# Optimization experiments

Hardware: AMD Instinct MI355X
Metric: run time of the kernel (lower is better)

Reference implementation:

```python
import jax, jax.numpy as jnp
import numpy as np

B, T, C = 1024, 512, 48

def setup_inputs() -> dict:
    key = jax.random.key(0)
    k1, k2, k3 = jax.random.split(key, 3)
    potentials = jax.random.normal(k1, (B, T, C), dtype=jnp.float32)
    sequence_lengths = jax.random.randint(k2, (B, 1), 1, T).astype(jnp.int32)
    # layer weight: uniform initializer (keras default uniform is U[-0.05, 0.05])
    transitions = jax.random.uniform(k3, (C, C), dtype=jnp.float32, minval=-0.05, maxval=0.05)
    return {"potentials": potentials, "sequence_lengths": sequence_lengths, "transitions": transitions}

def reference(potentials, sequence_lengths, transitions):
    # Faithful jax port of tf.contrib.crf.crf_decode (Viterbi max-plus DP),
    # followed by one_hot as in CRFLayer.call (inference branch of in_train_phase).
    Bb, Tt, Cc = potentials.shape
    seq_len = sequence_lengths.reshape(-1)  # K.flatten

    def fwd_step(score, xs):
        # score: [B,C] viterbi scores at step t-1
        pot_t, t = xs
        total = score[:, :, None] + transitions[None]  # [B, C_prev, C_cur]
        bp = jnp.argmax(total, axis=1).astype(jnp.int32)  # [B,C] best prev tag
        new_score = jnp.max(total, axis=1) + pot_t        # [B,C]
        valid = (t < seq_len)[:, None]                    # mask steps past seq_len
        score = jnp.where(valid, new_score, score)
        bp = jnp.where(valid, bp, jnp.arange(Cc, dtype=jnp.int32)[None])
        return score, bp

    init = potentials[:, 0]                               # [B,C]
    xs = (jnp.swapaxes(potentials[:, 1:], 0, 1), jnp.arange(1, Tt))
    last_score, bps = jax.lax.scan(fwd_step, init, xs)    # bps: [T-1,B,C]

    last_tag = jnp.argmax(last_score, axis=-1).astype(jnp.int32)  # [B]

    def back_step(tag_next, bp):
        prev = jnp.take_along_axis(bp, tag_next[:, None], axis=1)[:, 0]
        return prev, tag_next

    first_tag, tags_rest = jax.lax.scan(back_step, last_tag, bps, reverse=True)
    tags = jnp.concatenate([first_tag[None], tags_rest], axis=0)  # [T,B]
    tags = jnp.swapaxes(tags, 0, 1)                               # [B,T]
    return jax.nn.one_hot(tags, Cc, dtype=potentials.dtype)       # [B,T,C]
```

## Files before the change

### kernel.cpp

```cpp
#include <hip/hip_runtime.h>

#define T_DIM 512
#define C_DIM 48
#define BPS   48
#define CH    4

#if __has_builtin(__builtin_amdgcn_readlane)
#define READLANE_I(v, l) __builtin_amdgcn_readlane((v), (l))
#else
#define READLANE_I(v, l) __shfl((v), (l), 64)
#endif

#if __has_builtin(__builtin_amdgcn_wave_barrier)
#define WAVE_SYNC() do { __asm__ __volatile__("" ::: "memory"); __builtin_amdgcn_wave_barrier(); } while (0)
#else
#define WAVE_SYNC() __asm__ __volatile__("" ::: "memory")
#endif

#define DPP_MAX_STEP(V_, CTRL_) do {                                          \
    int o_ = __builtin_amdgcn_update_dpp(__float_as_int(V_),                  \
                                         __float_as_int(V_),                  \
                                         (CTRL_), 0xF, 0xF, false);           \
    V_ = fmaxf(V_, __int_as_float(o_));                                       \
} while (0)

__device__ __forceinline__ float wave_max_f(float v) {
    DPP_MAX_STEP(v, 0x111);
    DPP_MAX_STEP(v, 0x112);
    DPP_MAX_STEP(v, 0x114);
    DPP_MAX_STEP(v, 0x118);
    DPP_MAX_STEP(v, 0x142);
    DPP_MAX_STEP(v, 0x143);
    return __int_as_float(READLANE_I(__float_as_int(v), 63));
}

__global__ __launch_bounds__(64) void crf_viterbi(
    const float* __restrict__ pot,
    const int*   __restrict__ seqlen,
    const float* __restrict__ trans,
    float*       __restrict__ out)
{
    const int b   = blockIdx.x;
    const int tid = threadIdx.x;
    const int jj  = (tid < C_DIM) ? tid : (C_DIM - 1);

    __shared__ __align__(16) float trl[C_DIM * C_DIM];
    __shared__ unsigned char bp[T_DIM * BPS];
    __shared__ __align__(4) unsigned char tags[T_DIM];
    __shared__ __align__(16) float fsc[64];

    const float* potb = pot + (size_t)b * (T_DIM * C_DIM);
    const int L   = seqlen[b];
    const int thi = L - 1;

    float tm = 0.0f;
    for (int i = tid; i < C_DIM * C_DIM; i += 64) {
        float v = trans[i];
        trl[i] = v;
        tm = fmaxf(tm, fabsf(v));
    }
    const float tmax = wave_max_f(tm);
    const float nC5 = -(5.0f * tmax + 1e-3f);
    const float nC2 = -(2.0f * tmax + 1e-3f);
    WAVE_SYNC();

    float ns = potb[jj];
    float vthr = wave_max_f(ns) + nC2;

    const float* pp = potb + jj;

    float pb[CH];
    float pmr[CH];
#pragma unroll
    for (int k = 0; k < CH; ++k) {
        int tt = 1 + k; if (tt > T_DIM - 1) tt = T_DIM - 1;
        pb[k] = pp[tt * C_DIM];
    }
#pragma unroll
    for (int k = 0; k < CH; ++k) pmr[k] = wave_max_f(pb[k]);

    for (int t0 = 1; t0 < L; t0 += CH) {
        float nb[CH];
#pragma unroll
        for (int k = 0; k < CH; ++k) {
            int tt = t0 + CH + k; if (tt > T_DIM - 1) tt = T_DIM - 1;
            nb[k] = pp[tt * C_DIM];
        }
#pragma unroll
        for (int k = 0; k < CH; ++k) {
            const int t = t0 + k;
            if (t >= L) break;
            unsigned long long mm =
                __ballot(ns >= vthr) & 0x0000FFFFFFFFFFFFull;
            if (!mm) mm = 0x0000FFFFFFFFFFFFull;
            int c = (int)__builtin_ctzll(mm); mm &= mm - 1;
            float s_c = __int_as_float(READLANE_I(__float_as_int(ns), c));
            float m  = s_c + trl[c * C_DIM + jj];
            int   wi = c;
            while (mm) {
                int c2 = (int)__builtin_ctzll(mm); mm &= mm - 1;
                float s2 = __int_as_float(READLANE_I(__float_as_int(ns), c2));
                float cv = s2 + trl[c2 * C_DIM + jj];
                bool g = cv > m;
                m  = g ? cv : m;
                wi = g ? c2 : wi;
            }
            bp[t * BPS + tid] = (unsigned char)wi;
            ns   = m + pb[k];
            vthr = (m + pmr[k]) + nC5;
        }
        float pmn[CH];
#pragma unroll
        for (int k = 0; k < CH; ++k) pmn[k] = wave_max_f(nb[k]);
#pragma unroll
        for (int k = 0; k < CH; ++k) { pb[k] = nb[k]; pmr[k] = pmn[k]; }
    }

    fsc[tid] = ns;
    WAVE_SYNC();
    __syncthreads();

    const float* fs = fsc;
    float bv = fs[0];
    int   bi = 0;
#pragma unroll
    for (int i = 1; i < C_DIM; ++i) {
        float v = fs[i];
        if (v > bv) { bv = v; bi = i; }
    }
    const int last_tag = __builtin_amdgcn_readfirstlane(bi);

    for (int t = L + tid; t < T_DIM; t += 64) tags[t] = (unsigned char)last_tag;

    int y = last_tag;
    for (int c0 = (thi >> 6) << 6; c0 >= 0; c0 -= 64) {
        int row[64];
#pragma unroll
        for (int k = 0; k < 64; ++k) row[k] = bp[(c0 + k) * BPS + jj];

        int vacc = 0;
#pragma unroll
        for (int k = 63; k >= 0; --k) {
            const int t = c0 + k;
            vacc = (tid == k) ? y : vacc;
            const int ynew = READLANE_I(row[k], y);
            if ((unsigned)(t - 1) < (unsigned)thi) y = ynew;
        }
        const int tk = c0 + tid;
        if (tk <= thi) tags[tk] = (unsigned char)(vacc & 0xff);
    }
    __syncthreads();

    if (tid < C_DIM) {
        const int r = tid / 12;
        const int q = tid - r * 12;
        const int cbase = q * 4;
        float* ob = out + (size_t)b * (T_DIM * C_DIM);
        for (int t0 = 0; t0 < T_DIM; t0 += 4) {
            const unsigned int tg4 = *(const unsigned int*)&tags[t0];
            const int mytag = (int)((tg4 >> (r * 8)) & 0xffu);
            float4 v;
            v.x = (cbase + 0 == mytag) ? 1.0f : 0.0f;
            v.y = (cbase + 1 == mytag) ? 1.0f : 0.0f;
            v.z = (cbase + 2 == mytag) ? 1.0f : 0.0f;
            v.w = (cbase + 3 == mytag) ? 1.0f : 0.0f;
            *(float4*)(ob + (size_t)(t0 + r) * C_DIM + cbase) = v;
        }
    }
}

extern "C" void kernel_launch(void* const* d_in, const int* in_sizes, int n_in,
                              void* d_out, int out_size, void* d_ws, size_t ws_size,
                              hipStream_t stream) {
    const float* pot    = (const float*)d_in[0];
    const int*   sl     = (const int*)d_in[1];
    const float* trans  = (const float*)d_in[2];
    float*       out    = (float*)d_out;
    const int B = in_sizes[1];
    crf_viterbi<<<B, 64, 0, stream>>>(pot, sl, trans, out);
}
```

Baseline: 289.4 us.

## Precompute Viterbi candidate sets from potential rows and unroll first four candidates

Builds the candidate-predecessor mask for each step from the previous step's potential row (row >= rowmax - 5*tmax) instead of from the running score, so the masks and transition gathers for a whole chunk can be computed ahead of the serial dependency chain. The first four candidates are evaluated branch-free with max3 and an argmin trick on (v-max) bits OR'd with the index, and only further candidates go through a loop. This shortens the serial per-step critical path, at the cost of possibly looser masks, and relies on a pruning bound whose correctness depends on the potential-based argument.

```diff
diff --git a/kernel.cpp b/kernel.cpp
--- a/kernel.cpp
+++ b/kernel.cpp
@@ -16,6 +16,18 @@
 #else
 #define WAVE_SYNC() __asm__ __volatile__("" ::: "memory")
 #endif
+
+__device__ __forceinline__ unsigned umin_(unsigned a, unsigned b) { return a < b ? a : b; }
+__device__ __forceinline__ float max3f(float a, float b, float c) {
+    float d;
+    asm("v_max3_f32 %0, %1, %2, %3" : "=v"(d) : "v"(a), "v"(b), "v"(c));
+    return d;
+}
+__device__ __forceinline__ unsigned min3u(unsigned a, unsigned b, unsigned c) {
+    unsigned d;
+    asm("v_min3_u32 %0, %1, %2, %3" : "=v"(d) : "v"(a), "v"(b), "v"(c));
+    return d;
+}
 
 #define DPP_MAX_STEP(V_, CTRL_) do {                                          \
     int o_ = __builtin_amdgcn_update_dpp(__float_as_int(V_),                  \
@@ -61,23 +73,19 @@
     }
     const float tmax = wave_max_f(tm);
     const float nC5 = -(5.0f * tmax + 1e-3f);
-    const float nC2 = -(2.0f * tmax + 1e-3f);
     WAVE_SYNC();
 
-    float ns = potb[jj];
-    float vthr = wave_max_f(ns) + nC2;
+    float ns   = potb[jj];
+    float prow = ns;
 
     const float* pp = potb + jj;
 
     float pb[CH];
-    float pmr[CH];
 #pragma unroll
     for (int k = 0; k < CH; ++k) {
         int tt = 1 + k; if (tt > T_DIM - 1) tt = T_DIM - 1;
         pb[k] = pp[tt * C_DIM];
     }
-#pragma unroll
-    for (int k = 0; k < CH; ++k) pmr[k] = wave_max_f(pb[k]);
 
     for (int t0 = 1; t0 < L; t0 += CH) {
         float nb[CH];
@@ -86,34 +94,64 @@
             int tt = t0 + CH + k; if (tt > T_DIM - 1) tt = T_DIM - 1;
             nb[k] = pp[tt * C_DIM];
         }
+
+        int   cs[CH][4];
+        float gv[CH][4];
+        unsigned long long rem[CH];
+#pragma unroll
+        for (int k = 0; k < CH; ++k) {
+            const float row = (k == 0) ? prow : pb[k - 1];
+            const float pm  = wave_max_f(row);
+            unsigned long long mk =
+                __ballot(row >= pm + nC5) & 0x0000FFFFFFFFFFFFull;
+            if (!mk) mk = 0x0000FFFFFFFFFFFFull;
+            const int c0 = (int)__builtin_ctzll(mk);
+            const unsigned long long m1 = mk & (mk - 1);
+            const int c1 = m1 ? (int)__builtin_ctzll(m1) : c0;
+            const unsigned long long m2 = m1 & (m1 - 1);
+            const int c2 = m2 ? (int)__builtin_ctzll(m2) : c1;
+            const unsigned long long m3 = m2 & (m2 - 1);
+            const int c3 = m3 ? (int)__builtin_ctzll(m3) : c2;
+            rem[k] = m3 & (m3 - 1);
+            cs[k][0] = c0; cs[k][1] = c1; cs[k][2] = c2; cs[k][3] = c3;
+            gv[k][0] = trl[c0 * C_DIM + jj];
+            gv[k][1] = trl[c1 * C_DIM + jj];
+            gv[k][2] = trl[c2 * C_DIM + jj];
+            gv[k][3] = trl[c3 * C_DIM + jj];
+        }
+
 #pragma unroll
         for (int k = 0; k < CH; ++k) {
             const int t = t0 + k;
             if (t >= L) break;
-            unsigned long long mm =
-                __ballot(ns >= vthr) & 0x0000FFFFFFFFFFFFull;
-            if (!mm) mm = 0x0000FFFFFFFFFFFFull;
-            int c = (int)__builtin_ctzll(mm); mm &= mm - 1;
-            float s_c = __int_as_float(READLANE_I(__float_as_int(ns), c));
-            float m  = s_c + trl[c * C_DIM + jj];
-            int   wi = c;
-            while (mm) {
-                int c2 = (int)__builtin_ctzll(mm); mm &= mm - 1;
-                float s2 = __int_as_float(READLANE_I(__float_as_int(ns), c2));
-                float cv = s2 + trl[c2 * C_DIM + jj];
-                bool g = cv > m;
-                m  = g ? cv : m;
-                wi = g ? c2 : wi;
+            const float s0 = __int_as_float(READLANE_I(__float_as_int(ns), cs[k][0]));
+            const float s1 = __int_as_float(READLANE_I(__float_as_int(ns), cs[k][1]));
+            const float s2 = __int_as_float(READLANE_I(__float_as_int(ns), cs[k][2]));
+            const float s3 = __int_as_float(READLANE_I(__float_as_int(ns), cs[k][3]));
+            const float v0 = s0 + gv[k][0];
+            const float v1 = s1 + gv[k][1];
+            const float v2 = s2 + gv[k][2];
+            const float v3 = s3 + gv[k][3];
+            const float mx4 = fmaxf(max3f(v0, v1, v2), v3);
+            float mx = mx4;
+            const unsigned u0 = __float_as_uint(v0 - mx4) | (unsigned)cs[k][0];
+            const unsigned u1 = __float_as_uint(v1 - mx4) | (unsigned)cs[k][1];
+            const unsigned u2 = __float_as_uint(v2 - mx4) | (unsigned)cs[k][2];
+            const unsigned u3 = __float_as_uint(v3 - mx4) | (unsigned)cs[k][3];
+            int wi = (int)umin_(min3u(u0, u1, u2), u3);
+            unsigned long long rr = rem[k];
+            while (rr) {
+                int c = (int)__builtin_ctzll(rr); rr &= rr - 1;
+                float s = __int_as_float(READLANE_I(__float_as_int(ns), c));
+                float cv = s + trl[c * C_DIM + jj];
+                if (cv > mx) { mx = cv; wi = c; }
             }
             bp[t * BPS + tid] = (unsigned char)wi;
-            ns   = m + pb[k];
-            vthr = (m + pmr[k]) + nC5;
-        }
-        float pmn[CH];
-#pragma unroll
-        for (int k = 0; k < CH; ++k) pmn[k] = wave_max_f(nb[k]);
-#pragma unroll
-        for (int k = 0; k < CH; ++k) { pb[k] = nb[k]; pmr[k] = pmn[k]; }
+            ns = mx + pb[k];
+        }
+        prow = pb[CH - 1];
+#pragma unroll
+        for (int k = 0; k < CH; ++k) pb[k] = nb[k];
     }
 
     fsc[tid] = ns;
```

New measurement: 299.2 us. 1.03x slower.

## Precompute per-step candidate predecessor sets from potentials to shorten Viterbi inner loop

Applied to the files above, without the earlier changes.

Adds a prepass that tiles each sequence's potentials through shared memory and, for every timestep, packs into two words the indices of previous tags whose potential lies within a transition-bounded margin of the row max. The recurrence then reads these candidates instead of issuing a ballot and a dynamic readlane loop each step. It evaluates at most 8 candidates with max3/min3 instructions and packed index tie-breaking, and falls back to a full 48-way scan when more tags qualify. This is meant to take the ballot, the serial candidate loop and the per-step wave max reductions off the dependent chain, at the cost of an extra full pass over the potentials and more shared memory. The pruning assumes the previous score is bounded by the previous potential plus the transition range. Tie-breaking by subtracting the max and OR-ing in the index could differ from the reference argmax when values are nearly equal.

```diff
diff --git a/kernel.cpp b/kernel.cpp
--- a/kernel.cpp
+++ b/kernel.cpp
@@ -4,6 +4,7 @@
 #define C_DIM 48
 #define BPS   48
 #define CH    4
+#define SPAD  50
 
 #if __has_builtin(__builtin_amdgcn_readlane)
 #define READLANE_I(v, l) __builtin_amdgcn_readlane((v), (l))
@@ -16,6 +17,21 @@
 #else
 #define WAVE_SYNC() __asm__ __volatile__("" ::: "memory")
 #endif
+
+__device__ __forceinline__ unsigned umin_(unsigned a, unsigned b) { return a < b ? a : b; }
+__device__ __forceinline__ float rlane_f(float x, int lane) {
+    return __int_as_float(READLANE_I(__float_as_int(x), lane));
+}
+__device__ __forceinline__ float max3f(float a, float b, float c) {
+    float d;
+    asm("v_max3_f32 %0, %1, %2, %3" : "=v"(d) : "v"(a), "v"(b), "v"(c));
+    return d;
+}
+__device__ __forceinline__ unsigned min3u(unsigned a, unsigned b, unsigned c) {
+    unsigned d;
+    asm("v_min3_u32 %0, %1, %2, %3" : "=v"(d) : "v"(a), "v"(b), "v"(c));
+    return d;
+}
 
 #define DPP_MAX_STEP(V_, CTRL_) do {                                          \
     int o_ = __builtin_amdgcn_update_dpp(__float_as_int(V_),                  \
@@ -23,7 +39,6 @@
                                          (CTRL_), 0xF, 0xF, false);           \
     V_ = fmaxf(V_, __int_as_float(o_));                                       \
 } while (0)
-
 __device__ __forceinline__ float wave_max_f(float v) {
     DPP_MAX_STEP(v, 0x111);
     DPP_MAX_STEP(v, 0x112);
@@ -45,9 +60,11 @@
     const int jj  = (tid < C_DIM) ? tid : (C_DIM - 1);
 
     __shared__ __align__(16) float trl[C_DIM * C_DIM];
-    __shared__ unsigned char bp[T_DIM * BPS];
+    __shared__ __align__(16) unsigned char bp[T_DIM * BPS];
     __shared__ __align__(4) unsigned char tags[T_DIM];
     __shared__ __align__(16) float fsc[64];
+    __shared__ unsigned candA[T_DIM];
+    __shared__ unsigned candB[T_DIM];
 
     const float* potb = pot + (size_t)b * (T_DIM * C_DIM);
     const int L   = seqlen[b];
@@ -61,59 +78,148 @@
     }
     const float tmax = wave_max_f(tm);
     const float nC5 = -(5.0f * tmax + 1e-3f);
-    const float nC2 = -(2.0f * tmax + 1e-3f);
     WAVE_SYNC();
 
+    {
+        float* scratch = (float*)bp;
+        for (int tile = 0; tile < T_DIM / 64; ++tile) {
+            const int t0 = tile * 64;
+            const float4* gp4 = (const float4*)(potb + t0 * C_DIM);
+#pragma unroll
+            for (int it = 0; it < 12; ++it) {
+                const int i4  = tid + it * 64;
+                const float4 g = gp4[i4];
+                const int row = i4 / 12;
+                const int e4  = (i4 - row * 12) * 4;
+                float* d = &scratch[row * SPAD + e4];
+                d[0] = g.x; d[1] = g.y; d[2] = g.z; d[3] = g.w;
+            }
+            WAVE_SYNC();
+            const float2* r2 = (const float2*)&scratch[tid * SPAD];
+            float rmax = -__builtin_huge_valf();
+#pragma unroll
+            for (int q = 0; q < 24; ++q) {
+                const float2 v2 = r2[q];
+                rmax = fmaxf(rmax, fmaxf(v2.x, v2.y));
+            }
+            const float thr = rmax + nC5;
+            int cnt = 0;
+            int c0 = 0, c1 = 0, c2 = 0, c3 = 0, c4 = 0, c5 = 0, c6 = 0, c7 = 0;
+#pragma unroll
+            for (int q = 0; q < 24; ++q) {
+                const float2 v2 = r2[q];
+                {
+                    const bool tk = (v2.x >= thr); const int e = 2 * q;
+                    c0 = (tk && cnt == 0) ? e : c0;  c1 = (tk && cnt == 1) ? e : c1;
+                    c2 = (tk && cnt == 2) ? e : c2;  c3 = (tk && cnt == 3) ? e : c3;
+                    c4 = (tk && cnt == 4) ? e : c4;  c5 = (tk && cnt == 5) ? e : c5;
+                    c6 = (tk && cnt == 6) ? e : c6;  c7 = (tk && cnt == 7) ? e : c7;
+                    cnt += tk ? 1 : 0;
+                }
+                {
+                    const bool tk = (v2.y >= thr); const int e = 2 * q + 1;
+                    c0 = (tk && cnt == 0) ? e : c0;  c1 = (tk && cnt == 1) ? e : c1;
+                    c2 = (tk && cnt == 2) ? e : c2;  c3 = (tk && cnt == 3) ? e : c3;
+                    c4 = (tk && cnt == 4) ? e : c4;  c5 = (tk && cnt == 5) ? e : c5;
+                    c6 = (tk && cnt == 6) ? e : c6;  c7 = (tk && cnt == 7) ? e : c7;
+                    cnt += tk ? 1 : 0;
+                }
+            }
+            c1 = (cnt >= 2) ? c1 : c0;  c2 = (cnt >= 3) ? c2 : c1;
+            c3 = (cnt >= 4) ? c3 : c2;  c4 = (cnt >= 5) ? c4 : c3;
+            c5 = (cnt >= 6) ? c5 : c4;  c6 = (cnt >= 7) ? c6 : c5;
+            c7 = (cnt >= 8) ? c7 : c6;
+            const unsigned cc = (unsigned)(cnt > 15 ? 15 : cnt);
+            const unsigned aU = (unsigned)c0 | ((unsigned)c1 << 6) |
+                                ((unsigned)c2 << 12) | ((unsigned)c3 << 18) | (cc << 28);
+            const unsigned bU = (unsigned)c4 | ((unsigned)c5 << 6) |
+                                ((unsigned)c6 << 12) | ((unsigned)c7 << 18);
+            const int tt = t0 + tid + 1;
+            if (tt < T_DIM) { candA[tt] = aU; candB[tt] = bU; }
+            WAVE_SYNC();
+        }
+    }
+
     float ns = potb[jj];
-    float vthr = wave_max_f(ns) + nC2;
-
     const float* pp = potb + jj;
 
     float pb[CH];
-    float pmr[CH];
+    unsigned curA[CH], curB[CH];
 #pragma unroll
     for (int k = 0; k < CH; ++k) {
         int tt = 1 + k; if (tt > T_DIM - 1) tt = T_DIM - 1;
-        pb[k] = pp[tt * C_DIM];
-    }
-#pragma unroll
-    for (int k = 0; k < CH; ++k) pmr[k] = wave_max_f(pb[k]);
+        pb[k]   = pp[tt * C_DIM];
+        curA[k] = candA[tt];
+        curB[k] = candB[tt];
+    }
 
     for (int t0 = 1; t0 < L; t0 += CH) {
-        float nb[CH];
+        float nb[CH]; unsigned nxA[CH], nxB[CH];
 #pragma unroll
         for (int k = 0; k < CH; ++k) {
             int tt = t0 + CH + k; if (tt > T_DIM - 1) tt = T_DIM - 1;
-            nb[k] = pp[tt * C_DIM];
+            nb[k]  = pp[tt * C_DIM];
+            nxA[k] = candA[tt];
+            nxB[k] = candB[tt];
         }
 #pragma unroll
         for (int k = 0; k < CH; ++k) {
             const int t = t0 + k;
             if (t >= L) break;
-            unsigned long long mm =
-                __ballot(ns >= vthr) & 0x0000FFFFFFFFFFFFull;
-            if (!mm) mm = 0x0000FFFFFFFFFFFFull;
-            int c = (int)__builtin_ctzll(mm); mm &= mm - 1;
-            float s_c = __int_as_float(READLANE_I(__float_as_int(ns), c));
-            float m  = s_c + trl[c * C_DIM + jj];
-            int   wi = c;
-            while (mm) {
-                int c2 = (int)__builtin_ctzll(mm); mm &= mm - 1;
-                float s2 = __int_as_float(READLANE_I(__float_as_int(ns), c2));
-                float cv = s2 + trl[c2 * C_DIM + jj];
-                bool g = cv > m;
-                m  = g ? cv : m;
-                wi = g ? c2 : wi;
+            const unsigned aU = (unsigned)__builtin_amdgcn_readfirstlane((int)curA[k]);
+            const int cnt = (int)(aU >> 28);
+            const int cs0 = (int)(aU & 63u), cs1 = (int)((aU >> 6) & 63u);
+            const int cs2 = (int)((aU >> 12) & 63u), cs3 = (int)((aU >> 18) & 63u);
+            float mx; int wi;
+            if (cnt <= 8) {
+                const float s0 = rlane_f(ns, cs0), s1 = rlane_f(ns, cs1);
+                const float s2 = rlane_f(ns, cs2), s3 = rlane_f(ns, cs3);
+                const float v0 = s0 + trl[cs0 * C_DIM + jj];
+                const float v1 = s1 + trl[cs1 * C_DIM + jj];
+                const float v2 = s2 + trl[cs2 * C_DIM + jj];
+                const float v3 = s3 + trl[cs3 * C_DIM + jj];
+                if (cnt <= 4) {
+                    mx = fmaxf(max3f(v0, v1, v2), v3);
+                    const unsigned u0 = __float_as_uint(v0 - mx) | (unsigned)cs0;
+                    const unsigned u1 = __float_as_uint(v1 - mx) | (unsigned)cs1;
+                    const unsigned u2 = __float_as_uint(v2 - mx) | (unsigned)cs2;
+                    const unsigned u3 = __float_as_uint(v3 - mx) | (unsigned)cs3;
+                    wi = (int)umin_(min3u(u0, u1, u2), u3);
+                } else {
+                    const unsigned bU = (unsigned)__builtin_amdgcn_readfirstlane((int)curB[k]);
+                    const int cs4 = (int)(bU & 63u), cs5 = (int)((bU >> 6) & 63u);
+                    const int cs6 = (int)((bU >> 12) & 63u), cs7 = (int)((bU >> 18) & 63u);
+                    const float s4 = rlane_f(ns, cs4), s5 = rlane_f(ns, cs5);
+                    const float s6 = rlane_f(ns, cs6), s7 = rlane_f(ns, cs7);
+                    const float v4 = s4 + trl[cs4 * C_DIM + jj];
+                    const float v5 = s5 + trl[cs5 * C_DIM + jj];
+                    const float v6 = s6 + trl[cs6 * C_DIM + jj];
+                    const float v7 = s7 + trl[cs7 * C_DIM + jj];
+                    mx = fmaxf(fmaxf(max3f(v0, v1, v2), max3f(v3, v4, v5)), fmaxf(v6, v7));
+                    const unsigned u0 = __float_as_uint(v0 - mx) | (unsigned)cs0;
+                    const unsigned u1 = __float_as_uint(v1 - mx) | (unsigned)cs1;
+                    const unsigned u2 = __float_as_uint(v2 - mx) | (unsigned)cs2;
+                    const unsigned u3 = __float_as_uint(v3 - mx) | (unsigned)cs3;
+                    const unsigned u4 = __float_as_uint(v4 - mx) | (unsigned)cs4;
+                    const unsigned u5 = __float_as_uint(v5 - mx) | (unsigned)cs5;
+                    const unsigned u6 = __float_as_uint(v6 - mx) | (unsigned)cs6;
+                    const unsigned u7 = __float_as_uint(v7 - mx) | (unsigned)cs7;
+                    wi = (int)umin_(umin_(min3u(u0, u1, u2), min3u(u3, u4, u5)),
+                                    umin_(u6, u7));
+                }
+            } else {
+                mx = rlane_f(ns, 0) + trl[jj]; wi = 0;
+#pragma unroll 1
+                for (int i = 1; i < C_DIM; ++i) {
+                    const float v = rlane_f(ns, i) + trl[i * C_DIM + jj];
+                    if (v > mx) { mx = v; wi = i; }
+                }
             }
             bp[t * BPS + tid] = (unsigned char)wi;
-            ns   = m + pb[k];
-            vthr = (m + pmr[k]) + nC5;
-        }
-        float pmn[CH];
-#pragma unroll
-        for (int k = 0; k < CH; ++k) pmn[k] = wave_max_f(nb[k]);
-#pragma unroll
-        for (int k = 0; k < CH; ++k) { pb[k] = nb[k]; pmr[k] = pmn[k]; }
+            ns = mx + pb[k];
+        }
+#pragma unroll
+        for (int k = 0; k < CH; ++k) { pb[k] = nb[k]; curA[k] = nxA[k]; curB[k] = nxB[k]; }
     }
 
     fsc[tid] = ns;
```

Result: slower. 324.3 us (+12.1%).
